# Kernel tuning notes

Measured on AMD Instinct MI355X. Metric: run time of the kernel, lower is better.

## Reference

```python
import jax, jax.numpy as jnp
import numpy as np

B, S, IN, H, L, HEM, HTR = 128, 256, 88, 400, 100, 100, 200


def _lin(x, W, b):
    return x @ W.T + b


def setup_inputs() -> dict:
    key = jax.random.key(0)
    ks = iter(jax.random.split(key, 64))
    def p(shape, scale=0.05):
        return jax.random.normal(next(ks), shape, dtype=jnp.float32) * scale
    inp = {
        "x": jax.random.uniform(next(ks), (B, S, IN), dtype=jnp.float32),
        # bidirectional tanh RNN (1 layer)
        "Wih_f": p((H, IN)), "Whh_f": p((H, H)), "bih_f": p((H,)), "bhh_f": p((H,)),
        "Wih_b": p((H, IN)), "Whh_b": p((H, H)), "bih_b": p((H,)), "bhh_b": p((H,)),
        # DKS combiner
        "Wc": p((H, L)), "bc": p((H,)),
        "Wmu": p((L, H)), "bmu": p((L,)),
        "Wsig": p((L, H)), "bsig": p((L,)),
        # emission MLP
        "We1": p((HEM, L)), "be1": p((HEM,)),
        "We2": p((HEM, HEM)), "be2": p((HEM,)),
        "We3": p((IN, HEM)), "be3": p((IN,)),
        # gate G
        "Wg1": p((HTR, L)), "bg1": p((HTR,)),
        "Wg2": p((L, HTR)), "bg2": p((L,)),
        # proposed mean H
        "Wh1": p((HTR, L)), "bh1": p((HTR,)),
        "Wh2": p((L, HTR)), "bh2": p((L,)),
        # gated linear mu (init: identity weight, zero bias)
        "Wmg": jnp.eye(L, dtype=jnp.float32), "bmg": jnp.zeros((L,), jnp.float32),
        "Wsg": p((L, L)), "bsg": p((L,)),
        # pre-drawn sampling noise (stands in for torch.randn_like)
        "noise_inf": jax.random.normal(next(ks), (S, B, L), dtype=jnp.float32),
        "z0_gen": jax.random.normal(next(ks), (B, L), dtype=jnp.float32),
        "noise_gen": jax.random.normal(next(ks), (S, B, L), dtype=jnp.float32),
    }
    return inp


def _forward(x, Wih_f, Whh_f, bih_f, bhh_f, Wih_b, Whh_b, bih_b, bhh_b,
             Wc, bc, Wmu, bmu, Wsig, bsig,
             We1, be1, We2, be2, We3, be3,
             Wg1, bg1, Wg2, bg2, Wh1, bh1, Wh2, bh2, Wmg, bmg, Wsg, bsg,
             noise_inf, z0_gen, noise_gen):
    Bs = x.shape[0]
    # ---- bidirectional tanh RNN (batch_first) ----
    xf = (x @ Wih_f.T + bih_f).transpose(1, 0, 2)  # [S,B,H]
    xb = (x @ Wih_b.T + bih_b).transpose(1, 0, 2)

    def rnn_step_f(h, xt):
        h = jnp.tanh(xt + h @ Whh_f.T + bhh_f)
        return h, h

    def rnn_step_b(h, xt):
        h = jnp.tanh(xt + h @ Whh_b.T + bhh_b)
        return h, h

    h0 = jnp.zeros((Bs, H), x.dtype)
    _, out_f = jax.lax.scan(rnn_step_f, h0, xf)                 # [S,B,H] forward dir
    _, out_b_rev = jax.lax.scan(rnn_step_b, h0, xb[::-1])       # backward dir
    h_right = out_b_rev[::-1]                                   # [S,B,H], time-aligned
    # (h_left = out_f unused for combiner_type='dks')

    # ---- DKS combiner: sequential latent sampling ----
    def comb_step(z_prev, inp):
        hr_t, n_t = inp
        h = 0.5 * (jnp.tanh(z_prev @ Wc.T + bc) + hr_t)
        mu = h @ Wmu.T + bmu
        var = jax.nn.softplus(h @ Wsig.T + bsig)
        z_t = mu + jnp.sqrt(var) * n_t
        return z_t, (z_t, mu, var)

    z0 = jnp.zeros((Bs, L), x.dtype)
    _, (Z, mus_inf, sigmas_inf) = jax.lax.scan(comb_step, z0, (h_right, noise_inf))
    Z = Z.transpose(1, 0, 2)                 # [B,S,L]
    mus_inf = mus_inf.transpose(1, 0, 2)
    sigmas_inf = sigmas_inf.transpose(1, 0, 2)

    # ---- decoder emission (vectorized over B,S) ----
    e = jax.nn.relu(_lin(Z, We1, be1))
    e = jax.nn.relu(_lin(e, We2, be2))
    x_hat = jax.nn.sigmoid(_lin(e, We3, be3))  # [B,S,IN]

    # ---- decoder transition prior (sequential, self-driven) ----
    def tr_step(z_prev, n_t):
        g = jax.nn.sigmoid(jax.nn.relu(z_prev @ Wg1.T + bg1) @ Wg2.T + bg2)
        h_prop = jax.nn.relu(z_prev @ Wh1.T + bh1) @ Wh2.T + bh2
        mu = h_prop * g + (z_prev @ Wmg.T + bmg) * (1.0 - g)
        sigma = jax.nn.softplus(jax.nn.relu(h_prop) @ Wsg.T + bsg)
        z_t = mu + jnp.sqrt(sigma) * n_t
        return z_t, (mu, sigma)

    _, (mus_gen, sigmas_gen) = jax.lax.scan(tr_step, z0_gen, noise_gen)
    mus_gen = mus_gen.transpose(1, 0, 2)
    sigmas_gen = sigmas_gen.transpose(1, 0, 2)

    return (x_hat, mus_inf, sigmas_inf, mus_gen, sigmas_gen)


def reference(x, Wih_f, Whh_f, bih_f, bhh_f, Wih_b, Whh_b, bih_b, bhh_b,
              Wc, bc, Wmu, bmu, Wsig, bsig,
              We1, be1, We2, be2, We3, be3,
              Wg1, bg1, Wg2, bg2, Wh1, bh1, Wh2, bh2, Wmg, bmg, Wsg, bsg,
              noise_inf, z0_gen, noise_gen):
    return _forward(x, Wih_f, Whh_f, bih_f, bhh_f, Wih_b, Whh_b, bih_b, bhh_b,
                    Wc, bc, Wmu, bmu, Wsig, bsig,
                    We1, be1, We2, be2, We3, be3,
                    Wg1, bg1, Wg2, bg2, Wh1, bh1, Wh2, bh2, Wmg, bmg, Wsg, bsg,
                    noise_inf, z0_gen, noise_gen)
```

## Files before the change

kernel.cpp:

```cpp
#include <hip/hip_runtime.h>
#include <math.h>

typedef float f32x4 __attribute__((ext_vector_type(4)));
typedef short s16x8 __attribute__((ext_vector_type(8)));
typedef unsigned short u16;

#define DI __device__ __forceinline__

DI float bf2f(u16 h) { union { unsigned u; float f; } v; v.u = ((unsigned)h) << 16; return v.f; }
DI u16 f2bf(float f) {
  union { float f; unsigned u; } v; v.f = f;
  unsigned u = v.u;
  u += 0x7FFFu + ((u >> 16) & 1u);
  return (u16)(u >> 16);
}
DI float tanh_fast(float x) {
  float e = __expf(2.f * x);
  return 1.f - 2.f / (e + 1.f);
}
DI float sigmoid_f(float x) { return 1.f / (1.f + __expf(-x)); }
DI float softplus_f(float x) { return fmaxf(x, 0.f) + log1pf(__expf(-fabsf(x))); }
DI f32x4 mfma16(s16x8 a, s16x8 b, f32x4 c) {
  return __builtin_amdgcn_mfma_f32_16x16x32_bf16(a, b, c, 0, 0, 0);
}
DI void bar_lds() { asm volatile("s_waitcnt lgkmcnt(0)\n\ts_barrier" ::: "memory"); }

static constexpr size_t U_RNN = 0;
static constexpr size_t U_C1  = 186368;
static constexpr size_t U_C2  = 243712;
static constexpr size_t U_GA  = 336896;
static constexpr size_t U_GB  = 394240;
static constexpr size_t U_GC  = 444416;
static constexpr size_t U_E1  = 473088;
static constexpr size_t U_E2  = 487424;
static constexpr size_t U_E3  = 501760;
static constexpr size_t U_IN  = 514048;
static constexpr size_t U_XB  = 552448;
static constexpr size_t U_HR  = 13659648;

__global__ void k_pack(u16* __restrict__ ws,
    const float* __restrict__ Whh_b, const float* __restrict__ Wc,
    const float* __restrict__ Wmu, const float* __restrict__ Wsig,
    const float* __restrict__ Wg1, const float* __restrict__ Wh1,
    const float* __restrict__ Wg2, const float* __restrict__ Wh2,
    const float* __restrict__ Wmg, const float* __restrict__ Wsg,
    const float* __restrict__ We1, const float* __restrict__ We2,
    const float* __restrict__ We3, const float* __restrict__ Wih_b)
{
  int r = blockIdx.x, l = threadIdx.x;
  int region, local;
  if      (r < 364)  { region = 0; local = r; }
  else if (r < 476)  { region = 1; local = r - 364; }
  else if (r < 658)  { region = 2; local = r - 476; }
  else if (r < 770)  { region = 3; local = r - 658; }
  else if (r < 868)  { region = 4; local = r - 770; }
  else if (r < 924)  { region = 5; local = r - 868; }
  else if (r < 952)  { region = 6; local = r - 924; }
  else if (r < 980)  { region = 7; local = r - 952; }
  else if (r < 1004) { region = 8; local = r - 980; }
  else               { region = 9; local = r - 1004; }

  int NT; size_t base;
  switch (region) {
    case 0: NT = 28; base = U_RNN; break;
    case 1: NT = 28; base = U_C1;  break;
    case 2: NT = 14; base = U_C2;  break;
    case 3: NT = 28; base = U_GA;  break;
    case 4: NT = 14; base = U_GB;  break;
    case 5: NT = 14; base = U_GC;  break;
    case 6: NT = 7;  base = U_E1;  break;
    case 7: NT = 7;  base = U_E2;  break;
    case 8: NT = 6;  base = U_E3;  break;
    default:NT = 25; base = U_IN;  break;
  }
  int kt = local / NT, nt = local % NT;
  u16* out = ws + base + ((size_t)local * 64 + l) * 8;
  #pragma unroll
  for (int e = 0; e < 8; ++e) {
    int k = kt * 32 + (l >> 4) * 8 + e;
    int n = nt * 16 + (l & 15);
    float v = 0.f;
    switch (region) {
      case 0: if (n < 400 && k < 400) v = Whh_b[n * 400 + k]; break;
      case 1: if (n < 400 && k < 100) v = Wc[n * 100 + k]; break;
      case 2: if (n < 112) { if (n < 100 && k < 400) v = Wmu[n * 400 + k]; }
              else { int m = n - 112; if (m < 100 && k < 400) v = Wsig[m * 400 + k]; } break;
      case 3: if (n < 208) { if (n < 200 && k < 100) v = Wg1[n * 100 + k]; }
              else if (n < 416) { int m = n - 208; if (m < 200 && k < 100) v = Wh1[m * 100 + k]; } break;
      case 4: if (n < 112) { if (n < 100 && k < 200) v = Wg2[n * 200 + k]; }
              else { int m = n - 112; if (m < 100 && k < 200) v = Wh2[m * 200 + k]; } break;
      case 5: if (n < 112) { if (n < 100 && k < 100) v = Wmg[n * 100 + k]; }
              else { int m = n - 112; if (m < 100 && k < 100) v = Wsg[m * 100 + k]; } break;
      case 6: if (n < 100 && k < 100) v = We1[n * 100 + k]; break;
      case 7: if (n < 100 && k < 100) v = We2[n * 100 + k]; break;
      case 8: if (n < 88  && k < 100) v = We3[n * 100 + k]; break;
      default:if (n < 400 && k < 88)  v = Wih_b[n * 88 + k]; break;
    }
    out[e] = f2bf(v);
  }
}

__global__ __launch_bounds__(256) void k_proj(
    const float* __restrict__ x, const float* __restrict__ bih_b,
    const u16* __restrict__ pk_in, u16* __restrict__ xb)
{
  __shared__ __align__(16) u16 x_lds[16][104];
  const int tid = threadIdx.x;
  const int c = blockIdx.x;
  const int b = c >> 4, s0 = (c & 15) << 4;
  const float* xg = x + (size_t)c * 16 * 88;
  for (int idx = tid; idx < 16 * 104; idx += 256) {
    int r = idx / 104, k = idx % 104;
    x_lds[r][k] = (k < 88) ? f2bf(xg[r * 88 + k]) : (u16)0;
  }
  __syncthreads();
  const int w = tid >> 6, l = tid & 63, g = l >> 4, li = l & 15;
  s16x8 a[3];
  #pragma unroll
  for (int kt = 0; kt < 3; ++kt)
    a[kt] = *(const s16x8*)&x_lds[li][kt * 32 + g * 8];
  for (int nt = w; nt < 25; nt += 4) {
    f32x4 acc = (f32x4){0.f, 0.f, 0.f, 0.f};
    #pragma unroll
    for (int kt = 0; kt < 3; ++kt) {
      s16x8 bfr = *(const s16x8*)(pk_in + ((size_t)(kt * 25 + nt) * 64 + l) * 8);
      acc = mfma16(a[kt], bfr, acc);
    }
    int i = nt * 16 + li;
    float bias = bih_b[i];
    #pragma unroll
    for (int q = 0; q < 4; ++q) {
      int r = g * 4 + q;
      xb[((size_t)(s0 + r) * 128 + b) * 400 + i] = f2bf(acc[q] + bias);
    }
  }
}

__global__ __launch_bounds__(448) void k_scan(
    const u16* __restrict__ pk_rnn, const u16* __restrict__ pk_gA,
    const u16* __restrict__ pk_gB, const u16* __restrict__ pk_gC,
    const u16* __restrict__ xb, u16* __restrict__ hr, const float* __restrict__ bhh_b,
    const float* __restrict__ z0g, const float* __restrict__ bg1, const float* __restrict__ bh1,
    const float* __restrict__ bg2, const float* __restrict__ bh2,
    const float* __restrict__ bmg, const float* __restrict__ bsg,
    const float* __restrict__ noise_gen, float* __restrict__ mug, float* __restrict__ sgg)
{
  __shared__ __align__(16) u16 sm[69120];
  const int tid = threadIdx.x;
  const int w = tid >> 6, l = tid & 63, g = l >> 4, li = l & 15;
  const int bid = blockIdx.x;

  if (bid < 8) {
    u16* slab = sm;
    u16* hbuf = sm + 43008;
    for (int idx = tid; idx < 2 * 6784; idx += 448) hbuf[idx] = 0;
    {
      const uint4* src = (const uint4*)(pk_rnn + (size_t)10 * 28 * 512);
      uint4* dst = (uint4*)slab;
      for (int idx = tid; idx < 5376; idx += 448) dst[idx] = src[idx];
    }
    s16x8 wf[4][10];
    #pragma unroll
    for (int nt_l = 0; nt_l < 4; ++nt_l) {
      int nt = w * 4 + nt_l;
      #pragma unroll
      for (int kt = 0; kt < 10; ++kt)
        wf[nt_l][kt] = *(const s16x8*)(pk_rnn + ((size_t)(kt * 28 + nt) * 64 + l) * 8);
    }
    bool nv[4]; float bias_r[4];
    #pragma unroll
    for (int nt_l = 0; nt_l < 4; ++nt_l) {
      int n = (w * 4 + nt_l) * 16 + li;
      nv[nt_l] = (n < 400);
      bias_r[nt_l] = nv[nt_l] ? bhh_b[n] : 0.f;
    }
    const int b0 = bid * 16;
    u16 pf[4][4];
    #pragma unroll
    for (int nt_l = 0; nt_l < 4; ++nt_l) {
      if (nv[nt_l]) {
        int n = (w * 4 + nt_l) * 16 + li;
        #pragma unroll
        for (int q = 0; q < 4; ++q)
          pf[nt_l][q] = xb[((size_t)255 * 128 + b0 + g * 4 + q) * 400 + n];
      }
    }
    __syncthreads();
    int cur = 0;
    for (int t = 0; t < 256; ++t) {
      const int tt = 255 - t;
      f32x4 acc[4];
      #pragma unroll
      for (int i = 0; i < 4; ++i) acc[i] = (f32x4){0.f, 0.f, 0.f, 0.f};
      const u16* hb = hbuf + cur * 6784;
      #pragma unroll
      for (int kt = 0; kt < 13; ++kt) {
        s16x8 a = *(const s16x8*)(hb + li * 424 + kt * 32 + g * 8);
        if (kt < 10) {
          #pragma unroll
          for (int nt_l = 0; nt_l < 4; ++nt_l) acc[nt_l] = mfma16(a, wf[nt_l][kt], acc[nt_l]);
        } else {
          #pragma unroll
          for (int nt_l = 0; nt_l < 4; ++nt_l) {
            s16x8 bfr = *(const s16x8*)(slab + ((size_t)((kt - 10) * 28 + w * 4 + nt_l) * 64 + l) * 8);
            acc[nt_l] = mfma16(a, bfr, acc[nt_l]);
          }
        }
      }
      u16* hn = hbuf + (cur ^ 1) * 6784;
      #pragma unroll
      for (int nt_l = 0; nt_l < 4; ++nt_l) {
        if (nv[nt_l]) {
          int n = (w * 4 + nt_l) * 16 + li;
          #pragma unroll
          for (int q = 0; q < 4; ++q) {
            int r = g * 4 + q;
            float v = acc[nt_l][q] + bf2f(pf[nt_l][q]) + bias_r[nt_l];
            u16 hv = f2bf(tanh_fast(v));
            hn[r * 424 + n] = hv;
            hr[((size_t)tt * 128 + b0 + r) * 400 + n] = hv;
          }
        }
      }
      if (t < 255) {
        #pragma unroll
        for (int nt_l = 0; nt_l < 4; ++nt_l) {
          if (nv[nt_l]) {
            int n = (w * 4 + nt_l) * 16 + li;
            #pragma unroll
            for (int q = 0; q < 4; ++q)
              pf[nt_l][q] = xb[((size_t)(tt - 1) * 128 + b0 + g * 4 + q) * 400 + n];
          }
        }
      }
      bar_lds();
      cur ^= 1;
    }
  } else {
    u16* wA  = sm;
    u16* t1b = sm + 57344;
    u16* t2b = sm + 61056;
    u16* zb  = sm + 64768;
    u16* rhb = sm + 66944;
    const int b0 = (bid - 8) * 16;
    {
      const uint4* src = (const uint4*)pk_gA;
      uint4* dst = (uint4*)wA;
      for (int idx = tid; idx < 7168; idx += 448) dst[idx] = src[idx];
    }
    for (int idx = tid; idx < 2 * 3712; idx += 448) t1b[idx] = 0;
    for (int idx = tid; idx < 2176; idx += 448) {
      int r = idx / 136, c = idx % 136;
      zb[idx] = (c < 100) ? f2bf(z0g[(b0 + r) * 100 + c]) : (u16)0;
    }
    for (int idx = tid; idx < 2176; idx += 448) rhb[idx] = 0;

    s16x8 wBg[7], wBh[7], wCm[4], wCs[4];
    #pragma unroll
    for (int kt = 0; kt < 7; ++kt) {
      wBg[kt] = *(const s16x8*)(pk_gB + ((size_t)(kt * 14 + w) * 64 + l) * 8);
      wBh[kt] = *(const s16x8*)(pk_gB + ((size_t)(kt * 14 + 7 + w) * 64 + l) * 8);
    }
    #pragma unroll
    for (int kt = 0; kt < 4; ++kt) {
      wCm[kt] = *(const s16x8*)(pk_gC + ((size_t)(kt * 14 + w) * 64 + l) * 8);
      wCs[kt] = *(const s16x8*)(pk_gC + ((size_t)(kt * 14 + 7 + w) * 64 + l) * 8);
    }
    const int c = w * 16 + li;
    const bool cv = (c < 100);
    const float bg2_c = cv ? bg2[c] : 0.f;
    const float bh2_c = cv ? bh2[c] : 0.f;
    const float bmg_c = cv ? bmg[c] : 0.f;
    const float bsg_c = cv ? bsg[c] : 0.f;
    float b1r[4];
    #pragma unroll
    for (int nt_l = 0; nt_l < 4; ++nt_l) {
      int n = (w * 4 + nt_l) * 16 + li;
      bool is1 = n < 208;
      int j = is1 ? n : n - 208;
      b1r[nt_l] = (n < 416 && j < 200) ? (is1 ? bg1[j] : bh1[j]) : 0.f;
    }
    float pfn[4];
    #pragma unroll
    for (int q = 0; q < 4; ++q)
      pfn[q] = cv ? noise_gen[((size_t)0 * 128 + b0 + g * 4 + q) * 100 + c] : 0.f;
    __syncthreads();

    for (int t = 0; t < 256; ++t) {
      s16x8 az[4];
      #pragma unroll
      for (int kt = 0; kt < 4; ++kt)
        az[kt] = *(const s16x8*)(zb + li * 136 + kt * 32 + g * 8);
      {
        f32x4 a1[4];
        #pragma unroll
        for (int i = 0; i < 4; ++i) a1[i] = (f32x4){0.f, 0.f, 0.f, 0.f};
        #pragma unroll
        for (int kt = 0; kt < 4; ++kt) {
          #pragma unroll
          for (int nt_l = 0; nt_l < 4; ++nt_l) {
            s16x8 bfr = *(const s16x8*)(wA + ((size_t)(kt * 28 + w * 4 + nt_l) * 64 + l) * 8);
            a1[nt_l] = mfma16(az[kt], bfr, a1[nt_l]);
          }
        }
        #pragma unroll
        for (int nt_l = 0; nt_l < 4; ++nt_l) {
          int n = (w * 4 + nt_l) * 16 + li;
          if (n < 416) {
            bool is1 = n < 208;
            int j = is1 ? n : n - 208;
            u16* dst = is1 ? t1b : t2b;
            #pragma unroll
            for (int q = 0; q < 4; ++q)
              dst[(g * 4 + q) * 232 + j] = f2bf(fmaxf(a1[nt_l][q] + b1r[nt_l], 0.f));
          }
        }
      }
      bar_lds();
      float muq[4];
      {
        f32x4 ag = (f32x4){0.f,0.f,0.f,0.f}, ah = ag, am = ag;
        #pragma unroll
        for (int kt = 0; kt < 7; ++kt) {
          s16x8 x1 = *(const s16x8*)(t1b + li * 232 + kt * 32 + g * 8);
          ag = mfma16(x1, wBg[kt], ag);
        }
        #pragma unroll
        for (int kt = 0; kt < 7; ++kt) {
          s16x8 x2 = *(const s16x8*)(t2b + li * 232 + kt * 32 + g * 8);
          ah = mfma16(x2, wBh[kt], ah);
        }
        #pragma unroll
        for (int kt = 0; kt < 4; ++kt) am = mfma16(az[kt], wCm[kt], am);
        #pragma unroll
        for (int q = 0; q < 4; ++q) {
          int r = g * 4 + q;
          float gv = sigmoid_f(ag[q] + bg2_c);
          float hp = ah[q] + bh2_c;
          float m0 = am[q] + bmg_c;
          muq[q] = hp * gv + m0 * (1.f - gv);
          rhb[r * 136 + c] = f2bf(fmaxf(hp, 0.f));
          if (cv) mug[((size_t)(b0 + r) * 256 + t) * 100 + c] = muq[q];
        }
      }
      bar_lds();
      {
        f32x4 as = (f32x4){0.f,0.f,0.f,0.f};
        #pragma unroll
        for (int kt = 0; kt < 4; ++kt) {
          s16x8 xr = *(const s16x8*)(rhb + li * 136 + kt * 32 + g * 8);
          as = mfma16(xr, wCs[kt], as);
        }
        #pragma unroll
        for (int q = 0; q < 4; ++q) {
          int r = g * 4 + q;
          float sg = softplus_f(as[q] + bsg_c);
          if (cv) {
            sgg[((size_t)(b0 + r) * 256 + t) * 100 + c] = sg;
            zb[r * 136 + c] = f2bf(muq[q] + sqrtf(sg) * pfn[q]);
          }
        }
      }
      if (t < 255) {
        #pragma unroll
        for (int q = 0; q < 4; ++q)
          if (cv) pfn[q] = noise_gen[((size_t)(t + 1) * 128 + b0 + g * 4 + q) * 100 + c];
      }
      bar_lds();
    }
  }
}

__global__ __launch_bounds__(448) void k_comb(
    const u16* __restrict__ pk_c1, const u16* __restrict__ pk_c2,
    const u16* __restrict__ hr, const float* __restrict__ bc,
    const float* __restrict__ bmu, const float* __restrict__ bsig,
    const float* __restrict__ noise_inf,
    u16* __restrict__ Zws, float* __restrict__ mui, float* __restrict__ sgi)
{
  __shared__ __align__(16) u16 sm[66304];
  u16* wc1 = sm;
  u16* hb  = sm + 57344;
  u16* zb  = sm + 64128;
  const int tid = threadIdx.x;
  const int w = tid >> 6, l = tid & 63, g = l >> 4, li = l & 15;
  const int b0 = blockIdx.x * 16;

  {
    const uint4* src = (const uint4*)pk_c1;
    uint4* dst = (uint4*)wc1;
    for (int idx = tid; idx < 7168; idx += 448) dst[idx] = src[idx];
  }
  for (int idx = tid; idx < 6784 + 2176; idx += 448) hb[idx] = 0;

  s16x8 wMu[13], wSg[13];
  #pragma unroll
  for (int kt = 0; kt < 13; ++kt) {
    wMu[kt] = *(const s16x8*)(pk_c2 + ((size_t)(kt * 14 + w) * 64 + l) * 8);
    wSg[kt] = *(const s16x8*)(pk_c2 + ((size_t)(kt * 14 + 7 + w) * 64 + l) * 8);
  }
  const int c = w * 16 + li;
  const bool cv = (c < 100);
  const float bmu_c = cv ? bmu[c] : 0.f;
  const float bsig_c = cv ? bsig[c] : 0.f;
  bool nv[4]; float bc_r[4];
  #pragma unroll
  for (int nt_l = 0; nt_l < 4; ++nt_l) {
    int n = (w * 4 + nt_l) * 16 + li;
    nv[nt_l] = (n < 400);
    bc_r[nt_l] = nv[nt_l] ? bc[n] : 0.f;
  }
  u16 pf_hr[4][4];
  #pragma unroll
  for (int nt_l = 0; nt_l < 4; ++nt_l) {
    if (nv[nt_l]) {
      int n = (w * 4 + nt_l) * 16 + li;
      #pragma unroll
      for (int q = 0; q < 4; ++q)
        pf_hr[nt_l][q] = hr[((size_t)0 * 128 + b0 + g * 4 + q) * 400 + n];
    }
  }
  float pf_nz[4];
  #pragma unroll
  for (int q = 0; q < 4; ++q)
    pf_nz[q] = cv ? noise_inf[((size_t)0 * 128 + b0 + g * 4 + q) * 100 + c] : 0.f;
  __syncthreads();

  for (int t = 0; t < 256; ++t) {
    {
      s16x8 az[4];
      #pragma unroll
      for (int kt = 0; kt < 4; ++kt)
        az[kt] = *(const s16x8*)(zb + li * 136 + kt * 32 + g * 8);
      f32x4 a1[4];
      #pragma unroll
      for (int i = 0; i < 4; ++i) a1[i] = (f32x4){0.f, 0.f, 0.f, 0.f};
      #pragma unroll
      for (int kt = 0; kt < 4; ++kt) {
        #pragma unroll
        for (int nt_l = 0; nt_l < 4; ++nt_l) {
          s16x8 bfr = *(const s16x8*)(wc1 + ((size_t)(kt * 28 + w * 4 + nt_l) * 64 + l) * 8);
          a1[nt_l] = mfma16(az[kt], bfr, a1[nt_l]);
        }
      }
      #pragma unroll
      for (int nt_l = 0; nt_l < 4; ++nt_l) {
        if (nv[nt_l]) {
          int n = (w * 4 + nt_l) * 16 + li;
          #pragma unroll
          for (int q = 0; q < 4; ++q) {
            int r = g * 4 + q;
            float hv = 0.5f * (tanh_fast(a1[nt_l][q] + bc_r[nt_l]) + bf2f(pf_hr[nt_l][q]));
            hb[r * 424 + n] = f2bf(hv);
          }
        }
      }
      if (t < 255) {
        #pragma unroll
        for (int nt_l = 0; nt_l < 4; ++nt_l) {
          if (nv[nt_l]) {
            int n = (w * 4 + nt_l) * 16 + li;
            #pragma unroll
            for (int q = 0; q < 4; ++q)
              pf_hr[nt_l][q] = hr[((size_t)(t + 1) * 128 + b0 + g * 4 + q) * 400 + n];
          }
        }
      }
    }
    bar_lds();
    {
      f32x4 am = (f32x4){0.f,0.f,0.f,0.f}, as = am;
      #pragma unroll
      for (int kt = 0; kt < 13; ++kt) {
        s16x8 a = *(const s16x8*)(hb + li * 424 + kt * 32 + g * 8);
        am = mfma16(a, wMu[kt], am);
        as = mfma16(a, wSg[kt], as);
      }
      #pragma unroll
      for (int q = 0; q < 4; ++q) {
        int r = g * 4 + q;
        float mu = am[q] + bmu_c;
        float va = softplus_f(as[q] + bsig_c);
        if (cv) {
          size_t o = ((size_t)(b0 + r) * 256 + t) * 100 + c;
          mui[o] = mu;
          sgi[o] = va;
          float z = mu + sqrtf(va) * pf_nz[q];
          zb[r * 136 + c] = f2bf(z);
          Zws[((size_t)(b0 + r) * 256 + t) * 112 + c] = f2bf(z);
        }
      }
      if (t < 255) {
        #pragma unroll
        for (int q = 0; q < 4; ++q)
          if (cv) pf_nz[q] = noise_inf[((size_t)(t + 1) * 128 + b0 + g * 4 + q) * 100 + c];
      }
    }
    bar_lds();
  }
}

__global__ __launch_bounds__(448) void k_dec(
    const u16* __restrict__ Zws,
    const u16* __restrict__ pk_e1, const u16* __restrict__ pk_e2, const u16* __restrict__ pk_e3,
    const float* __restrict__ be1, const float* __restrict__ be2, const float* __restrict__ be3,
    float* __restrict__ xh)
{
  __shared__ __align__(16) u16 sm[3 * 2176];
  u16* zb = sm; u16* e1b = sm + 2176; u16* e2b = sm + 4352;
  const int tid = threadIdx.x;
  const int w = tid >> 6, l = tid & 63, g = l >> 4, li = l & 15;
  const int cc = blockIdx.x;
  const int b = cc >> 4, s0 = (cc & 15) << 4;

  s16x8 w1[4], w2[4], w3[4];
  #pragma unroll
  for (int kt = 0; kt < 4; ++kt) {
    w1[kt] = *(const s16x8*)(pk_e1 + ((size_t)(kt * 7 + w) * 64 + l) * 8);
    w2[kt] = *(const s16x8*)(pk_e2 + ((size_t)(kt * 7 + w) * 64 + l) * 8);
    if (w < 6) w3[kt] = *(const s16x8*)(pk_e3 + ((size_t)(kt * 6 + w) * 64 + l) * 8);
  }
  {
    const uint4* zsrc = (const uint4*)(Zws + ((size_t)b * 256 + s0) * 112);
    for (int idx = tid; idx < 224; idx += 448) {
      int r = idx / 14, cj = idx % 14;
      *(uint4*)(zb + r * 136 + cj * 8) = zsrc[idx];
    }
    for (int idx = tid; idx < 3 * 384; idx += 448) {
      int bi = idx / 384, j = idx % 384;
      (sm + bi * 2176)[(j / 24) * 136 + 112 + (j % 24)] = 0;
    }
  }
  __syncthreads();
  const int c = w * 16 + li;
  {
    f32x4 acc = (f32x4){0.f,0.f,0.f,0.f};
    #pragma unroll
    for (int kt = 0; kt < 4; ++kt) {
      s16x8 a = *(const s16x8*)(zb + li * 136 + kt * 32 + g * 8);
      acc = mfma16(a, w1[kt], acc);
    }
    float bias = (c < 100) ? be1[c] : 0.f;
    #pragma unroll
    for (int q = 0; q < 4; ++q)
      e1b[(g * 4 + q) * 136 + c] = f2bf(fmaxf(acc[q] + bias, 0.f));
  }
  bar_lds();
  {
    f32x4 acc = (f32x4){0.f,0.f,0.f,0.f};
    #pragma unroll
    for (int kt = 0; kt < 4; ++kt) {
      s16x8 a = *(const s16x8*)(e1b + li * 136 + kt * 32 + g * 8);
      acc = mfma16(a, w2[kt], acc);
    }
    float bias = (c < 100) ? be2[c] : 0.f;
    #pragma unroll
    for (int q = 0; q < 4; ++q)
      e2b[(g * 4 + q) * 136 + c] = f2bf(fmaxf(acc[q] + bias, 0.f));
  }
  bar_lds();
  if (w < 6) {
    f32x4 acc = (f32x4){0.f,0.f,0.f,0.f};
    #pragma unroll
    for (int kt = 0; kt < 4; ++kt) {
      s16x8 a = *(const s16x8*)(e2b + li * 136 + kt * 32 + g * 8);
      acc = mfma16(a, w3[kt], acc);
    }
    int n = w * 16 + li;
    if (n < 88) {
      float bias = be3[n];
      #pragma unroll
      for (int q = 0; q < 4; ++q)
        xh[((size_t)b * 256 + s0 + g * 4 + q) * 88 + n] = sigmoid_f(acc[q] + bias);
    }
  }
}

extern "C" void kernel_launch(void* const* d_in, const int* in_sizes, int n_in,
                              void* d_out, int out_size, void* d_ws, size_t ws_size,
                              hipStream_t stream) {
  const float* x      = (const float*)d_in[0];
  const float* Wih_b  = (const float*)d_in[5];
  const float* Whh_b  = (const float*)d_in[6];
  const float* bih_b  = (const float*)d_in[7];
  const float* bhh_b  = (const float*)d_in[8];
  const float* Wc     = (const float*)d_in[9];
  const float* bc     = (const float*)d_in[10];
  const float* Wmu    = (const float*)d_in[11];
  const float* bmu    = (const float*)d_in[12];
  const float* Wsig   = (const float*)d_in[13];
  const float* bsig   = (const float*)d_in[14];
  const float* We1    = (const float*)d_in[15];
  const float* be1    = (const float*)d_in[16];
  const float* We2    = (const float*)d_in[17];
  const float* be2    = (const float*)d_in[18];
  const float* We3    = (const float*)d_in[19];
  const float* be3    = (const float*)d_in[20];
  const float* Wg1    = (const float*)d_in[21];
  const float* bg1    = (const float*)d_in[22];
  const float* Wg2    = (const float*)d_in[23];
  const float* bg2    = (const float*)d_in[24];
  const float* Wh1    = (const float*)d_in[25];
  const float* bh1    = (const float*)d_in[26];
  const float* Wh2    = (const float*)d_in[27];
  const float* bh2    = (const float*)d_in[28];
  const float* Wmg    = (const float*)d_in[29];
  const float* bmg    = (const float*)d_in[30];
  const float* Wsg    = (const float*)d_in[31];
  const float* bsg    = (const float*)d_in[32];
  const float* noise_inf = (const float*)d_in[33];
  const float* z0_gen    = (const float*)d_in[34];
  const float* noise_gen = (const float*)d_in[35];

  u16* ws16 = (u16*)d_ws;
  float* out = (float*)d_out;
  float* xh  = out;
  float* mui = out + 2883584;
  float* sgi = out + 6160384;
  float* mug = out + 9437184;
  float* sgg = out + 12713984;
  u16* Zws = ws16 + U_XB;

  k_pack<<<1079, 64, 0, stream>>>(ws16, Whh_b, Wc, Wmu, Wsig, Wg1, Wh1, Wg2, Wh2,
                                  Wmg, Wsg, We1, We2, We3, Wih_b);
  k_proj<<<2048, 256, 0, stream>>>(x, bih_b, ws16 + U_IN, ws16 + U_XB);
  k_scan<<<16, 448, 0, stream>>>(ws16 + U_RNN, ws16 + U_GA, ws16 + U_GB, ws16 + U_GC,
                                 ws16 + U_XB, ws16 + U_HR, bhh_b,
                                 z0_gen, bg1, bh1, bg2, bh2, bmg, bsg, noise_gen, mug, sgg);
  k_comb<<<8, 448, 0, stream>>>(ws16 + U_C1, ws16 + U_C2, ws16 + U_HR, bc, bmu, bsig,
                                noise_inf, Zws, mui, sgi);
  k_dec<<<2048, 448, 0, stream>>>(Zws, ws16 + U_E1, ws16 + U_E2, ws16 + U_E3,
                                  be1, be2, be3, xh);
}
```

Before: 2.070 ms.

## Fuse combiner scan into RNN scan blocks with shared per-thread slot layout

```diff
diff --git a/kernel.cpp b/kernel.cpp
--- a/kernel.cpp
+++ b/kernel.cpp
@@ -24,6 +24,9 @@
   return __builtin_amdgcn_mfma_f32_16x16x32_bf16(a, b, c, 0, 0, 0);
 }
 DI void bar_lds() { asm volatile("s_waitcnt lgkmcnt(0)\n\ts_barrier" ::: "memory"); }
+DI int fa(int k, int row) { return ((k >> 5) << 9) + ((((k >> 3) & 3) * 16 + row) << 3) + (k & 7); }
+
+union P16 { uint4 v[2]; u16 u[16]; };
 
 static constexpr size_t U_RNN = 0;
 static constexpr size_t U_C1  = 186368;
@@ -35,8 +38,7 @@
 static constexpr size_t U_E2  = 487424;
 static constexpr size_t U_E3  = 501760;
 static constexpr size_t U_IN  = 514048;
-static constexpr size_t U_XB  = 552448;
-static constexpr size_t U_HR  = 13659648;
+static constexpr size_t U_SL  = 552448;
 
 __global__ void k_pack(u16* __restrict__ ws,
     const float* __restrict__ Whh_b, const float* __restrict__ Wc,
@@ -102,19 +104,20 @@
 
 __global__ __launch_bounds__(256) void k_proj(
     const float* __restrict__ x, const float* __restrict__ bih_b,
-    const u16* __restrict__ pk_in, u16* __restrict__ xb)
+    const u16* __restrict__ pk_in, u16* __restrict__ slot)
 {
   __shared__ __align__(16) u16 x_lds[16][104];
   const int tid = threadIdx.x;
-  const int c = blockIdx.x;
-  const int b = c >> 4, s0 = (c & 15) << 4;
-  const float* xg = x + (size_t)c * 16 * 88;
+  const int cblk = blockIdx.x;
+  const int b = cblk >> 4, s0 = (cblk & 15) << 4;
+  const float* xg = x + (size_t)cblk * 16 * 88;
   for (int idx = tid; idx < 16 * 104; idx += 256) {
     int r = idx / 104, k = idx % 104;
     x_lds[r][k] = (k < 88) ? f2bf(xg[r * 88 + k]) : (u16)0;
   }
   __syncthreads();
   const int w = tid >> 6, l = tid & 63, g = l >> 4, li = l & 15;
+  const int bid2 = b >> 4, r2 = b & 15, g2 = r2 >> 2, q2 = r2 & 3;
   s16x8 a[3];
   #pragma unroll
   for (int kt = 0; kt < 3; ++kt)
@@ -128,134 +131,245 @@
     }
     int i = nt * 16 + li;
     float bias = bih_b[i];
+    int thr = ((i >> 6) << 6) + (g2 << 4) + (i & 15);
+    int elem = (((i >> 4) & 3) << 2) + q2;
     #pragma unroll
     for (int q = 0; q < 4; ++q) {
-      int r = g * 4 + q;
-      xb[((size_t)(s0 + r) * 128 + b) * 400 + i] = f2bf(acc[q] + bias);
+      int s = s0 + g * 4 + q;
+      slot[((size_t)(s * 8 + bid2) * 448 + thr) * 16 + elem] = f2bf(acc[q] + bias);
     }
   }
 }
 
 __global__ __launch_bounds__(448) void k_scan(
-    const u16* __restrict__ pk_rnn, const u16* __restrict__ pk_gA,
-    const u16* __restrict__ pk_gB, const u16* __restrict__ pk_gC,
-    const u16* __restrict__ xb, u16* __restrict__ hr, const float* __restrict__ bhh_b,
+    const u16* __restrict__ pk_rnn, const u16* __restrict__ pk_c1, const u16* __restrict__ pk_c2,
+    const u16* __restrict__ pk_gA, const u16* __restrict__ pk_gB, const u16* __restrict__ pk_gC,
+    u16* __restrict__ slot, const float* __restrict__ bhh_b,
+    const float* __restrict__ bc, const float* __restrict__ bmu, const float* __restrict__ bsig,
+    const float* __restrict__ noise_inf,
     const float* __restrict__ z0g, const float* __restrict__ bg1, const float* __restrict__ bh1,
     const float* __restrict__ bg2, const float* __restrict__ bh2,
     const float* __restrict__ bmg, const float* __restrict__ bsg,
-    const float* __restrict__ noise_gen, float* __restrict__ mug, float* __restrict__ sgg)
+    const float* __restrict__ noise_gen,
+    float* __restrict__ mui, float* __restrict__ sgi,
+    float* __restrict__ mug, float* __restrict__ sgg)
 {
-  __shared__ __align__(16) u16 sm[69120];
+  __shared__ __align__(16) u16 sm[56320];
   const int tid = threadIdx.x;
   const int w = tid >> 6, l = tid & 63, g = l >> 4, li = l & 15;
   const int bid = blockIdx.x;
 
+  {
+    uint4 z4 = (uint4){0, 0, 0, 0};
+    uint4* p = (uint4*)sm;
+    for (int idx = tid; idx < 7040; idx += 448) p[idx] = z4;
+  }
+  __syncthreads();
+
   if (bid < 8) {
-    u16* slab = sm;
-    u16* hbuf = sm + 43008;
-    for (int idx = tid; idx < 2 * 6784; idx += 448) hbuf[idx] = 0;
+    const int b0 = bid * 16;
     {
-      const uint4* src = (const uint4*)(pk_rnn + (size_t)10 * 28 * 512);
-      uint4* dst = (uint4*)slab;
-      for (int idx = tid; idx < 5376; idx += 448) dst[idx] = src[idx];
-    }
-    s16x8 wf[4][10];
-    #pragma unroll
-    for (int nt_l = 0; nt_l < 4; ++nt_l) {
-      int nt = w * 4 + nt_l;
-      #pragma unroll
-      for (int kt = 0; kt < 10; ++kt)
-        wf[nt_l][kt] = *(const s16x8*)(pk_rnn + ((size_t)(kt * 28 + nt) * 64 + l) * 8);
-    }
-    bool nv[4]; float bias_r[4];
-    #pragma unroll
-    for (int nt_l = 0; nt_l < 4; ++nt_l) {
-      int n = (w * 4 + nt_l) * 16 + li;
-      nv[nt_l] = (n < 400);
-      bias_r[nt_l] = nv[nt_l] ? bhh_b[n] : 0.f;
-    }
-    const int b0 = bid * 16;
-    u16 pf[4][4];
-    #pragma unroll
-    for (int nt_l = 0; nt_l < 4; ++nt_l) {
-      if (nv[nt_l]) {
+      u16* slab = sm;
+      u16* hbuf = sm + 43008;
+      {
+        const uint4* src = (const uint4*)(pk_rnn + (size_t)10 * 28 * 512);
+        uint4* dst = (uint4*)slab;
+        for (int idx = tid; idx < 5376; idx += 448) dst[idx] = src[idx];
+      }
+      s16x8 wf[4][10];
+      #pragma unroll
+      for (int nt_l = 0; nt_l < 4; ++nt_l) {
+        int nt = w * 4 + nt_l;
+        #pragma unroll
+        for (int kt = 0; kt < 10; ++kt)
+          wf[nt_l][kt] = *(const s16x8*)(pk_rnn + ((size_t)(kt * 28 + nt) * 64 + l) * 8);
+      }
+      bool nv[4]; float bias_r[4];
+      #pragma unroll
+      for (int nt_l = 0; nt_l < 4; ++nt_l) {
         int n = (w * 4 + nt_l) * 16 + li;
-        #pragma unroll
-        for (int q = 0; q < 4; ++q)
-          pf[nt_l][q] = xb[((size_t)255 * 128 + b0 + g * 4 + q) * 400 + n];
-      }
-    }
-    __syncthreads();
-    int cur = 0;
-    for (int t = 0; t < 256; ++t) {
-      const int tt = 255 - t;
-      f32x4 acc[4];
-      #pragma unroll
-      for (int i = 0; i < 4; ++i) acc[i] = (f32x4){0.f, 0.f, 0.f, 0.f};
-      const u16* hb = hbuf + cur * 6784;
-      #pragma unroll
-      for (int kt = 0; kt < 13; ++kt) {
-        s16x8 a = *(const s16x8*)(hb + li * 424 + kt * 32 + g * 8);
-        if (kt < 10) {
-          #pragma unroll
-          for (int nt_l = 0; nt_l < 4; ++nt_l) acc[nt_l] = mfma16(a, wf[nt_l][kt], acc[nt_l]);
-        } else {
-          #pragma unroll
-          for (int nt_l = 0; nt_l < 4; ++nt_l) {
-            s16x8 bfr = *(const s16x8*)(slab + ((size_t)((kt - 10) * 28 + w * 4 + nt_l) * 64 + l) * 8);
-            acc[nt_l] = mfma16(a, bfr, acc[nt_l]);
-          }
-        }
-      }
-      u16* hn = hbuf + (cur ^ 1) * 6784;
-      #pragma unroll
-      for (int nt_l = 0; nt_l < 4; ++nt_l) {
-        if (nv[nt_l]) {
-          int n = (w * 4 + nt_l) * 16 + li;
-          #pragma unroll
-          for (int q = 0; q < 4; ++q) {
-            int r = g * 4 + q;
-            float v = acc[nt_l][q] + bf2f(pf[nt_l][q]) + bias_r[nt_l];
-            u16 hv = f2bf(tanh_fast(v));
-            hn[r * 424 + n] = hv;
-            hr[((size_t)tt * 128 + b0 + r) * 400 + n] = hv;
-          }
-        }
-      }
-      if (t < 255) {
+        nv[nt_l] = (n < 400);
+        bias_r[nt_l] = nv[nt_l] ? bhh_b[n] : 0.f;
+      }
+      P16 pf;
+      {
+        size_t base = ((size_t)(255 * 8 + bid) * 448 + w * 64 + l) * 16;
+        pf.v[0] = *(const uint4*)(slot + base);
+        pf.v[1] = *(const uint4*)(slot + base + 8);
+      }
+      __syncthreads();
+      int cur = 0;
+      for (int t = 0; t < 256; ++t) {
+        const int tt = 255 - t;
+        f32x4 acc[4];
+        #pragma unroll
+        for (int i = 0; i < 4; ++i) acc[i] = (f32x4){0.f, 0.f, 0.f, 0.f};
+        const u16* hb = hbuf + cur * 6656;
+        #pragma unroll
+        for (int kt = 0; kt < 13; ++kt) {
+          s16x8 a = *(const s16x8*)(hb + kt * 512 + l * 8);
+          if (kt < 10) {
+            #pragma unroll
+            for (int nt_l = 0; nt_l < 4; ++nt_l) acc[nt_l] = mfma16(a, wf[nt_l][kt], acc[nt_l]);
+          } else {
+            #pragma unroll
+            for (int nt_l = 0; nt_l < 4; ++nt_l) {
+              s16x8 bfr = *(const s16x8*)(slab + ((size_t)((kt - 10) * 28 + w * 4 + nt_l) * 512) + l * 8);
+              acc[nt_l] = mfma16(a, bfr, acc[nt_l]);
+            }
+          }
+        }
+        u16* hn = hbuf + (cur ^ 1) * 6656;
+        P16 st; st.v[0] = (uint4){0,0,0,0}; st.v[1] = (uint4){0,0,0,0};
         #pragma unroll
         for (int nt_l = 0; nt_l < 4; ++nt_l) {
           if (nv[nt_l]) {
             int n = (w * 4 + nt_l) * 16 + li;
             #pragma unroll
+            for (int q = 0; q < 4; ++q) {
+              float v = acc[nt_l][q] + bf2f(pf.u[nt_l * 4 + q]) + bias_r[nt_l];
+              u16 hv = f2bf(tanh_fast(v));
+              hn[fa(n, 4 * g + q)] = hv;
+              st.u[nt_l * 4 + q] = hv;
+            }
+          }
+        }
+        {
+          size_t base = ((size_t)(tt * 8 + bid) * 448 + w * 64 + l) * 16;
+          *(uint4*)(slot + base) = st.v[0];
+          *(uint4*)(slot + base + 8) = st.v[1];
+        }
+        if (t < 255) {
+          size_t nb = ((size_t)((tt - 1) * 8 + bid) * 448 + w * 64 + l) * 16;
+          pf.v[0] = *(const uint4*)(slot + nb);
+          pf.v[1] = *(const uint4*)(slot + nb + 8);
+        }
+        bar_lds();
+        cur ^= 1;
+      }
+    }
+    __syncthreads();
+    {
+      u16* hbF = sm;
+      u16* zbF = sm + 6656;
+      for (int idx = tid; idx < 8704; idx += 448) sm[idx] = 0;
+      s16x8 wC1[4][4], wMu[13], wSg[13];
+      #pragma unroll
+      for (int nt_l = 0; nt_l < 4; ++nt_l) {
+        int nt = w * 4 + nt_l;
+        #pragma unroll
+        for (int kt = 0; kt < 4; ++kt)
+          wC1[nt_l][kt] = *(const s16x8*)(pk_c1 + ((size_t)(kt * 28 + nt) * 64 + l) * 8);
+      }
+      #pragma unroll
+      for (int kt = 0; kt < 13; ++kt) {
+        wMu[kt] = *(const s16x8*)(pk_c2 + ((size_t)(kt * 14 + w) * 64 + l) * 8);
+        wSg[kt] = *(const s16x8*)(pk_c2 + ((size_t)(kt * 14 + 7 + w) * 64 + l) * 8);
+      }
+      const int c = w * 16 + li;
+      const bool cv = (c < 100);
+      const float bmu_c = cv ? bmu[c] : 0.f;
+      const float bsig_c = cv ? bsig[c] : 0.f;
+      bool nv[4]; float bc_r[4];
+      #pragma unroll
+      for (int nt_l = 0; nt_l < 4; ++nt_l) {
+        int n = (w * 4 + nt_l) * 16 + li;
+        nv[nt_l] = (n < 400);
+        bc_r[nt_l] = nv[nt_l] ? bc[n] : 0.f;
+      }
+      P16 pf;
+      {
+        size_t base = ((size_t)(0 * 8 + bid) * 448 + w * 64 + l) * 16;
+        pf.v[0] = *(const uint4*)(slot + base);
+        pf.v[1] = *(const uint4*)(slot + base + 8);
+      }
+      float pf_nz[4];
+      #pragma unroll
+      for (int q = 0; q < 4; ++q)
+        pf_nz[q] = cv ? noise_inf[((size_t)0 * 128 + b0 + g * 4 + q) * 100 + c] : 0.f;
+      __syncthreads();
+
+      for (int t = 0; t < 256; ++t) {
+        {
+          s16x8 az[4];
+          #pragma unroll
+          for (int kt = 0; kt < 4; ++kt)
+            az[kt] = *(const s16x8*)(zbF + kt * 512 + l * 8);
+          f32x4 a1[4];
+          #pragma unroll
+          for (int i = 0; i < 4; ++i) a1[i] = (f32x4){0.f, 0.f, 0.f, 0.f};
+          #pragma unroll
+          for (int kt = 0; kt < 4; ++kt) {
+            #pragma unroll
+            for (int nt_l = 0; nt_l < 4; ++nt_l) a1[nt_l] = mfma16(az[kt], wC1[nt_l][kt], a1[nt_l]);
+          }
+          #pragma unroll
+          for (int nt_l = 0; nt_l < 4; ++nt_l) {
+            if (nv[nt_l]) {
+              int n = (w * 4 + nt_l) * 16 + li;
+              #pragma unroll
+              for (int q = 0; q < 4; ++q) {
+                float hv = 0.5f * (tanh_fast(a1[nt_l][q] + bc_r[nt_l]) + bf2f(pf.u[nt_l * 4 + q]));
+                hbF[fa(n, 4 * g + q)] = f2bf(hv);
+              }
+            }
+          }
+          if (t < 255) {
+            size_t nb = ((size_t)((t + 1) * 8 + bid) * 448 + w * 64 + l) * 16;
+            pf.v[0] = *(const uint4*)(slot + nb);
+            pf.v[1] = *(const uint4*)(slot + nb + 8);
+          }
+        }
+        bar_lds();
+        {
+          f32x4 am = (f32x4){0.f,0.f,0.f,0.f}, as_ = am;
+          #pragma unroll
+          for (int kt = 0; kt < 13; ++kt) {
+            s16x8 a = *(const s16x8*)(hbF + kt * 512 + l * 8);
+            am = mfma16(a, wMu[kt], am);
+            as_ = mfma16(a, wSg[kt], as_);
+          }
+          #pragma unroll
+          for (int q = 0; q < 4; ++q) {
+            int r = g * 4 + q;
+            float mu = am[q] + bmu_c;
+            float va = softplus_f(as_[q] + bsig_c);
+            if (cv) {
+              size_t o = ((size_t)(b0 + r) * 256 + t) * 100 + c;
+              mui[o] = mu;
+              sgi[o] = va;
+              float z = mu + sqrtf(va) * pf_nz[q];
+              zbF[fa(c, r)] = f2bf(z);
+              slot[(size_t)(t * 8 + bid) * 7168 + r * 112 + c] = f2bf(z);
+            }
+          }
+          if (t < 255) {
+            #pragma unroll
             for (int q = 0; q < 4; ++q)
-              pf[nt_l][q] = xb[((size_t)(tt - 1) * 128 + b0 + g * 4 + q) * 400 + n];
-          }
-        }
-      }
-      bar_lds();
-      cur ^= 1;
+              if (cv) pf_nz[q] = noise_inf[((size_t)(t + 1) * 128 + b0 + g * 4 + q) * 100 + c];
+          }
+        }
+        bar_lds();
+      }
     }
   } else {
-    u16* wA  = sm;
-    u16* t1b = sm + 57344;
-    u16* t2b = sm + 61056;
-    u16* zb  = sm + 64768;
-    u16* rhb = sm + 66944;
     const int b0 = (bid - 8) * 16;
-    {
-      const uint4* src = (const uint4*)pk_gA;
-      uint4* dst = (uint4*)wA;
-      for (int idx = tid; idx < 7168; idx += 448) dst[idx] = src[idx];
-    }
-    for (int idx = tid; idx < 2 * 3712; idx += 448) t1b[idx] = 0;
-    for (int idx = tid; idx < 2176; idx += 448) {
-      int r = idx / 136, c = idx % 136;
-      zb[idx] = (c < 100) ? f2bf(z0g[(b0 + r) * 100 + c]) : (u16)0;
-    }
-    for (int idx = tid; idx < 2176; idx += 448) rhb[idx] = 0;
-
-    s16x8 wBg[7], wBh[7], wCm[4], wCs[4];
+    u16* zbF  = sm;
+    u16* rhbF = sm + 2048;
+    u16* t1F  = sm + 4096;
+    u16* t2F  = sm + 7680;
+    for (int idx = tid; idx < 2048; idx += 448) {
+      int r = idx >> 7, c = idx & 127;
+      zbF[fa(c, r)] = (c < 100) ? f2bf(z0g[(b0 + r) * 100 + c]) : (u16)0;
+    }
+    s16x8 wA[4][4], wBg[7], wBh[7], wCm[4], wCs[4];
+    #pragma unroll
+    for (int nt_l = 0; nt_l < 4; ++nt_l) {
+      int nt = w * 4 + nt_l;
+      #pragma unroll
+      for (int kt = 0; kt < 4; ++kt)
+        wA[nt_l][kt] = *(const s16x8*)(pk_gA + ((size_t)(kt * 28 + nt) * 64 + l) * 8);
+    }
     #pragma unroll
     for (int kt = 0; kt < 7; ++kt) {
       wBg[kt] = *(const s16x8*)(pk_gB + ((size_t)(kt * 14 + w) * 64 + l) * 8);
@@ -290,7 +404,7 @@
       s16x8 az[4];
       #pragma unroll
       for (int kt = 0; kt < 4; ++kt)
-        az[kt] = *(const s16x8*)(zb + li * 136 + kt * 32 + g * 8);
+        az[kt] = *(const s16x8*)(zbF + kt * 512 + l * 8);
       {
         f32x4 a1[4];
         #pragma unroll
@@ -298,10 +412,7 @@
         #pragma unroll
         for (int kt = 0; kt < 4; ++kt) {
           #pragma unroll
-          for (int nt_l = 0; nt_l < 4; ++nt_l) {
-            s16x8 bfr = *(const s16x8*)(wA + ((size_t)(kt * 28 + w * 4 + nt_l) * 64 + l) * 8);
-            a1[nt_l] = mfma16(az[kt], bfr, a1[nt_l]);
-          }
+          for (int nt_l = 0; nt_l < 4; ++nt_l) a1[nt_l] = mfma16(az[kt], wA[nt_l][kt], a1[nt_l]);
         }
         #pragma unroll
         for (int nt_l = 0; nt_l < 4; ++nt_l) {
@@ -309,10 +420,10 @@
           if (n < 416) {
             bool is1 = n < 208;
             int j = is1 ? n : n - 208;
-            u16* dst = is1 ? t1b : t2b;
+            u16* dst = is1 ? t1F : t2F;
             #pragma unroll
             for (int q = 0; q < 4; ++q)
-              dst[(g * 4 + q) * 232 + j] = f2bf(fmaxf(a1[nt_l][q] + b1r[nt_l], 0.f));
+              dst[fa(j, 4 * g + q)] = f2bf(fmaxf(a1[nt_l][q] + b1r[nt_l], 0.f));
           }
         }
       }
@@ -322,12 +433,12 @@
         f32x4 ag = (f32x4){0.f,0.f,0.f,0.f}, ah = ag, am = ag;
         #pragma unroll
         for (int kt = 0; kt < 7; ++kt) {
-          s16x8 x1 = *(const s16x8*)(t1b + li * 232 + kt * 32 + g * 8);
+          s16x8 x1 = *(const s16x8*)(t1F + kt * 512 + l * 8);
           ag = mfma16(x1, wBg[kt], ag);
         }
         #pragma unroll
         for (int kt = 0; kt < 7; ++kt) {
-          s16x8 x2 = *(const s16x8*)(t2b + li * 232 + kt * 32 + g * 8);
+          s16x8 x2 = *(const s16x8*)(t2F + kt * 512 + l * 8);
           ah = mfma16(x2, wBh[kt], ah);
         }
         #pragma unroll
@@ -339,169 +450,40 @@
           float hp = ah[q] + bh2_c;
           float m0 = am[q] + bmg_c;
           muq[q] = hp * gv + m0 * (1.f - gv);
-          rhb[r * 136 + c] = f2bf(fmaxf(hp, 0.f));
+          rhbF[fa(c, r)] = f2bf(fmaxf(hp, 0.f));
           if (cv) mug[((size_t)(b0 + r) * 256 + t) * 100 + c] = muq[q];
         }
       }
       bar_lds();
       {
-        f32x4 as = (f32x4){0.f,0.f,0.f,0.f};
+        f32x4 as2 = (f32x4){0.f,0.f,0.f,0.f};
         #pragma unroll
         for (int kt = 0; kt < 4; ++kt) {
-          s16x8 xr = *(const s16x8*)(rhb + li * 136 + kt * 32 + g * 8);
-          as = mfma16(xr, wCs[kt], as);
+          s16x8 xr = *(const s16x8*)(rhbF + kt * 512 + l * 8);
+          as2 = mfma16(xr, wCs[kt], as2);
         }
         #pragma unroll
         for (int q = 0; q < 4; ++q) {
           int r = g * 4 + q;
-          float sg = softplus_f(as[q] + bsg_c);
+          float sg = softplus_f(as2[q] + bsg_c);
           if (cv) {
             sgg[((size_t)(b0 + r) * 256 + t) * 100 + c] = sg;
-            zb[r * 136 + c] = f2bf(muq[q] + sqrtf(sg) * pfn[q]);
-          }
-        }
-      }
-      if (t < 255) {
-        #pragma unroll
-        for (int q = 0; q < 4; ++q)
-          if (cv) pfn[q] = noise_gen[((size_t)(t + 1) * 128 + b0 + g * 4 + q) * 100 + c];
+            zbF[fa(c, r)] = f2bf(muq[q] + sqrtf(sg) * pfn[q]);
+          }
+        }
+        if (t < 255) {
+          #pragma unroll
+          for (int q = 0; q < 4; ++q)
+            if (cv) pfn[q] = noise_gen[((size_t)(t + 1) * 128 + b0 + g * 4 + q) * 100 + c];
+        }
       }
       bar_lds();
     }
   }
 }
 
-__global__ __launch_bounds__(448) void k_comb(
-    const u16* __restrict__ pk_c1, const u16* __restrict__ pk_c2,
-    const u16* __restrict__ hr, const float* __restrict__ bc,
-    const float* __restrict__ bmu, const float* __restrict__ bsig,
-    const float* __restrict__ noise_inf,
-    u16* __restrict__ Zws, float* __restrict__ mui, float* __restrict__ sgi)
-{
-  __shared__ __align__(16) u16 sm[66304];
-  u16* wc1 = sm;
-  u16* hb  = sm + 57344;
-  u16* zb  = sm + 64128;
-  const int tid = threadIdx.x;
-  const int w = tid >> 6, l = tid & 63, g = l >> 4, li = l & 15;
-  const int b0 = blockIdx.x * 16;
-
-  {
-    const uint4* src = (const uint4*)pk_c1;
-    uint4* dst = (uint4*)wc1;
-    for (int idx = tid; idx < 7168; idx += 448) dst[idx] = src[idx];
-  }
-  for (int idx = tid; idx < 6784 + 2176; idx += 448) hb[idx] = 0;
-
-  s16x8 wMu[13], wSg[13];
-  #pragma unroll
-  for (int kt = 0; kt < 13; ++kt) {
-    wMu[kt] = *(const s16x8*)(pk_c2 + ((size_t)(kt * 14 + w) * 64 + l) * 8);
-    wSg[kt] = *(const s16x8*)(pk_c2 + ((size_t)(kt * 14 + 7 + w) * 64 + l) * 8);
-  }
-  const int c = w * 16 + li;
-  const bool cv = (c < 100);
-  const float bmu_c = cv ? bmu[c] : 0.f;
-  const float bsig_c = cv ? bsig[c] : 0.f;
-  bool nv[4]; float bc_r[4];
-  #pragma unroll
-  for (int nt_l = 0; nt_l < 4; ++nt_l) {
-    int n = (w * 4 + nt_l) * 16 + li;
-    nv[nt_l] = (n < 400);
-    bc_r[nt_l] = nv[nt_l] ? bc[n] : 0.f;
-  }
-  u16 pf_hr[4][4];
-  #pragma unroll
-  for (int nt_l = 0; nt_l < 4; ++nt_l) {
-    if (nv[nt_l]) {
-      int n = (w * 4 + nt_l) * 16 + li;
-      #pragma unroll
-      for (int q = 0; q < 4; ++q)
-        pf_hr[nt_l][q] = hr[((size_t)0 * 128 + b0 + g * 4 + q) * 400 + n];
-    }
-  }
-  float pf_nz[4];
-  #pragma unroll
-  for (int q = 0; q < 4; ++q)
-    pf_nz[q] = cv ? noise_inf[((size_t)0 * 128 + b0 + g * 4 + q) * 100 + c] : 0.f;
-  __syncthreads();
-
-  for (int t = 0; t < 256; ++t) {
-    {
-      s16x8 az[4];
-      #pragma unroll
-      for (int kt = 0; kt < 4; ++kt)
-        az[kt] = *(const s16x8*)(zb + li * 136 + kt * 32 + g * 8);
-      f32x4 a1[4];
-      #pragma unroll
-      for (int i = 0; i < 4; ++i) a1[i] = (f32x4){0.f, 0.f, 0.f, 0.f};
-      #pragma unroll
-      for (int kt = 0; kt < 4; ++kt) {
-        #pragma unroll
-        for (int nt_l = 0; nt_l < 4; ++nt_l) {
-          s16x8 bfr = *(const s16x8*)(wc1 + ((size_t)(kt * 28 + w * 4 + nt_l) * 64 + l) * 8);
-          a1[nt_l] = mfma16(az[kt], bfr, a1[nt_l]);
-        }
-      }
-      #pragma unroll
-      for (int nt_l = 0; nt_l < 4; ++nt_l) {
-        if (nv[nt_l]) {
-          int n = (w * 4 + nt_l) * 16 + li;
-          #pragma unroll
-          for (int q = 0; q < 4; ++q) {
-            int r = g * 4 + q;
-            float hv = 0.5f * (tanh_fast(a1[nt_l][q] + bc_r[nt_l]) + bf2f(pf_hr[nt_l][q]));
-            hb[r * 424 + n] = f2bf(hv);
-          }
-        }
-      }
-      if (t < 255) {
-        #pragma unroll
-        for (int nt_l = 0; nt_l < 4; ++nt_l) {
-          if (nv[nt_l]) {
-            int n = (w * 4 + nt_l) * 16 + li;
-            #pragma unroll
-            for (int q = 0; q < 4; ++q)
-              pf_hr[nt_l][q] = hr[((size_t)(t + 1) * 128 + b0 + g * 4 + q) * 400 + n];
-          }
-        }
-      }
-    }
-    bar_lds();
-    {
-      f32x4 am = (f32x4){0.f,0.f,0.f,0.f}, as = am;
-      #pragma unroll
-      for (int kt = 0; kt < 13; ++kt) {
-        s16x8 a = *(const s16x8*)(hb + li * 424 + kt * 32 + g * 8);
-        am = mfma16(a, wMu[kt], am);
-        as = mfma16(a, wSg[kt], as);
-      }
-      #pragma unroll
-      for (int q = 0; q < 4; ++q) {
-        int r = g * 4 + q;
-        float mu = am[q] + bmu_c;
-        float va = softplus_f(as[q] + bsig_c);
-        if (cv) {
-          size_t o = ((size_t)(b0 + r) * 256 + t) * 100 + c;
-          mui[o] = mu;
-          sgi[o] = va;
-          float z = mu + sqrtf(va) * pf_nz[q];
-          zb[r * 136 + c] = f2bf(z);
-          Zws[((size_t)(b0 + r) * 256 + t) * 112 + c] = f2bf(z);
-        }
-      }
-      if (t < 255) {
-        #pragma unroll
-        for (int q = 0; q < 4; ++q)
-          if (cv) pf_nz[q] = noise_inf[((size_t)(t + 1) * 128 + b0 + g * 4 + q) * 100 + c];
-      }
-    }
-    bar_lds();
-  }
-}
-
 __global__ __launch_bounds__(448) void k_dec(
-    const u16* __restrict__ Zws,
+    const u16* __restrict__ slot,
     const u16* __restrict__ pk_e1, const u16* __restrict__ pk_e2, const u16* __restrict__ pk_e3,
     const float* __restrict__ be1, const float* __restrict__ be2, const float* __restrict__ be3,
     float* __restrict__ xh)
@@ -512,6 +494,7 @@
   const int w = tid >> 6, l = tid & 63, g = l >> 4, li = l & 15;
   const int cc = blockIdx.x;
   const int b = cc >> 4, s0 = (cc & 15) << 4;
+  const int bid2 = b >> 4, r2 = b & 15;
 
   s16x8 w1[4], w2[4], w3[4];
   #pragma unroll
@@ -521,10 +504,10 @@
     if (w < 6) w3[kt] = *(const s16x8*)(pk_e3 + ((size_t)(kt * 6 + w) * 64 + l) * 8);
   }
   {
-    const uint4* zsrc = (const uint4*)(Zws + ((size_t)b * 256 + s0) * 112);
     for (int idx = tid; idx < 224; idx += 448) {
       int r = idx / 14, cj = idx % 14;
-      *(uint4*)(zb + r * 136 + cj * 8) = zsrc[idx];
+      size_t src = ((size_t)((s0 + r) * 8 + bid2)) * 7168 + r2 * 112 + cj * 8;
+      *(uint4*)(zb + r * 136 + cj * 8) = *(const uint4*)(slot + src);
     }
     for (int idx = tid; idx < 3 * 384; idx += 448) {
       int bi = idx / 384, j = idx % 384;
@@ -619,16 +602,17 @@
   float* sgi = out + 6160384;
   float* mug = out + 9437184;
   float* sgg = out + 12713984;
-  u16* Zws = ws16 + U_XB;
+  u16* slot = ws16 + U_SL;
 
   k_pack<<<1079, 64, 0, stream>>>(ws16, Whh_b, Wc, Wmu, Wsig, Wg1, Wh1, Wg2, Wh2,
                                   Wmg, Wsg, We1, We2, We3, Wih_b);
-  k_proj<<<2048, 256, 0, stream>>>(x, bih_b, ws16 + U_IN, ws16 + U_XB);
-  k_scan<<<16, 448, 0, stream>>>(ws16 + U_RNN, ws16 + U_GA, ws16 + U_GB, ws16 + U_GC,
-                                 ws16 + U_XB, ws16 + U_HR, bhh_b,
-                                 z0_gen, bg1, bh1, bg2, bh2, bmg, bsg, noise_gen, mug, sgg);
-  k_comb<<<8, 448, 0, stream>>>(ws16 + U_C1, ws16 + U_C2, ws16 + U_HR, bc, bmu, bsig,
-                                noise_inf, Zws, mui, sgi);
-  k_dec<<<2048, 448, 0, stream>>>(Zws, ws16 + U_E1, ws16 + U_E2, ws16 + U_E3,
+  k_proj<<<2048, 256, 0, stream>>>(x, bih_b, ws16 + U_IN, slot);
+  k_scan<<<16, 448, 0, stream>>>(ws16 + U_RNN, ws16 + U_C1, ws16 + U_C2,
+                                 ws16 + U_GA, ws16 + U_GB, ws16 + U_GC,
+                                 slot, bhh_b,
+                                 bc, bmu, bsig, noise_inf,
+                                 z0_gen, bg1, bh1, bg2, bh2, bmg, bsg, noise_gen,
+                                 mui, sgi, mug, sgg);
+  k_dec<<<2048, 448, 0, stream>>>(slot, ws16 + U_E1, ws16 + U_E2, ws16 + U_E3,
                                   be1, be2, be3, xh);
 }
```

Result: faster. 1.775 ms (-14.2%).
